# Performance work log

Hardware: AMD Instinct MI355X
Metric: run time of the kernel (lower is better)

## Reference

```python
import jax, jax.numpy as jnp
import numpy as np

TEMPERATURE = 0.1  # use_temperature=True


def setup_inputs() -> dict:
    key = jax.random.key(0)
    # encoder output features: [batch_size, num_epoch, feature_dim]
    feature = jax.random.normal(key, (128, 64, 128), dtype=jnp.float32)
    return {"feature": feature}


def reference(feature):
    # L2-normalize along feature dim (F.normalize, p=2, dim=1 on flat features)
    f = feature / jnp.linalg.norm(feature, axis=-1, keepdims=True)
    B, E, D = f.shape
    # full pairwise logits: [B, E, E, B]
    logits = jnp.einsum('ijk,mnk->ijnm', f, f) / TEMPERATURE
    e = jnp.exp(logits)
    idx = jnp.arange(B)
    # mask[i, j, :, i] = 1 -> positives are the m == i block: e[i, j, :, i]
    pos = e[idx, :, :, idx].sum(-1)              # [B, E]
    neg = e.sum(axis=(2, 3)) - pos               # [B, E] everything else
    loss = (-jnp.log(pos / (pos + neg))).mean()
    return loss
```

## Files before the change

kernel.cpp:

```cpp
#include <hip/hip_runtime.h>
#include <hip/hip_bf16.h>

#define N_ROWS 8192
#define DIM    128
#define TILE   128
#define CPG    8
#define EXPTEN 22026.465794806718f
#define SCALE  3.7982826f

typedef __attribute__((ext_vector_type(8))) short short8;
typedef __attribute__((ext_vector_type(4))) float floatx4;

#define EXP2F(x) __builtin_amdgcn_exp2f(x)

#define GLOAD_LDS(g, l)                                                        \
    __builtin_amdgcn_global_load_lds(                                          \
        (const __attribute__((address_space(1))) void*)(g),                    \
        (__attribute__((address_space(3))) void*)(l), 16, 0, 0)

__global__ void norm_kernel(const float* __restrict__ F, __hip_bfloat16* __restrict__ Xb,
                            float* __restrict__ pos, float* __restrict__ den) {
    int lane = threadIdx.x & 63;
    int wave = threadIdx.x >> 6;
    int row  = blockIdx.x * 4 + wave;
    const float2 v = *(const float2*)(F + (size_t)row * DIM + lane * 2);
    float ss = v.x * v.x + v.y * v.y;
    #pragma unroll
    for (int m = 1; m < 64; m <<= 1) ss += __shfl_xor(ss, m);
    float inv = rsqrtf(ss) * SCALE;
    __hip_bfloat162 o;
    o.x = __float2bfloat16(v.x * inv);
    o.y = __float2bfloat16(v.y * inv);
    *((__hip_bfloat162*)(Xb + (size_t)row * DIM) + lane) = o;
    if (lane == 0) { pos[row] = 0.f; den[row] = 0.f; }
}

__global__ __launch_bounds__(256, 2) void gram_kernel(
        const __hip_bfloat16* __restrict__ Xb,
        float* __restrict__ pos, float* __restrict__ den) {
    __shared__ __hip_bfloat16 Bs[2][TILE * DIM];
    const int tid  = threadIdx.x;
    const int rb   = blockIdx.x;
    const int cg   = blockIdx.y;
    const int lane = tid & 63;
    const int wave = tid >> 6;
    const int wm   = wave >> 1, wn = wave & 1;
    const int quad = lane >> 4;
    const int l15  = lane & 15;

    short8 af[4][4];
    {
        const __hip_bfloat16* Ab = Xb + ((size_t)(rb * TILE + wm * 64 + l15)) * DIM + quad * 8;
        #pragma unroll
        for (int mi = 0; mi < 4; ++mi)
            #pragma unroll
            for (int ko = 0; ko < 4; ++ko)
                af[mi][ko] = *(const short8*)(Ab + mi * 16 * DIM + ko * 32);
    }

    float dp[4][4];
    #pragma unroll
    for (int a = 0; a < 4; ++a)
        #pragma unroll
        for (int b = 0; b < 4; ++b) dp[a][b] = 0.f;

    auto stage = [&](int ct, int buf) {
        #pragma unroll
        for (int i = 0; i < 8; ++i) {
            int chunk = (i * 4 + wave) * 64 + lane;
            int r  = chunk >> 4;
            int cs = (chunk & 15) ^ (r & 15);
            const __hip_bfloat16* gp = Xb + ((size_t)(ct * TILE + r)) * DIM + cs * 8;
            char* lp = (char*)&Bs[buf][0] + (i * 4 + wave) * 1024;
            GLOAD_LDS(gp, lp);
        }
    };

    auto compute = [&](int ct, int buf) {
        floatx4 acc[4][4];
        #pragma unroll
        for (int mi = 0; mi < 4; ++mi)
            #pragma unroll
            for (int ni = 0; ni < 4; ++ni) acc[mi][ni] = (floatx4)0.0f;

        const char* Bb = (const char*)&Bs[buf][0];
        #pragma unroll
        for (int ko = 0; ko < 4; ++ko) {
            short8 bf[4];
            #pragma unroll
            for (int ni = 0; ni < 4; ++ni) {
                int r  = wn * 64 + ni * 16 + l15;
                int ch = (ko * 4 + quad) ^ l15;
                bf[ni] = *(const short8*)(Bb + r * 256 + ch * 16);
            }
            #pragma unroll
            for (int mi = 0; mi < 4; ++mi)
                #pragma unroll
                for (int ni = 0; ni < 4; ++ni)
                    acc[mi][ni] = __builtin_amdgcn_mfma_f32_16x16x32_bf16(
                        af[mi][ko], bf[ni], acc[mi][ni], 0, 0, 0);
        }

        const bool pos_tile = (ct == rb) && (wm == wn);
        #pragma unroll
        for (int mi = 0; mi < 4; ++mi)
            #pragma unroll
            for (int rg = 0; rg < 4; ++rg) {
                float dadd = 0.f;
                #pragma unroll
                for (int ni = 0; ni < 4; ++ni)
                    dadd += EXP2F(acc[mi][ni][rg]);
                if (pos_tile) {
                    if (l15 == quad * 4 + rg)
                        dadd += EXPTEN - EXP2F(acc[mi][mi][rg]);
                    float p = dadd;
                    #pragma unroll
                    for (int m = 1; m < 16; m <<= 1) p += __shfl_xor(p, m);
                    if (l15 == 0)
                        atomicAdd(&pos[rb * TILE + wm * 64 + mi * 16 + quad * 4 + rg], p);
                }
                dp[mi][rg] += dadd;
            }
    };

    stage(cg * CPG, 0);
    __syncthreads();
    #pragma unroll 1
    for (int t = 0; t < CPG - 1; ++t) {
        stage(cg * CPG + t + 1, (t + 1) & 1);
        compute(cg * CPG + t, t & 1);
        __syncthreads();
    }
    compute(cg * CPG + CPG - 1, (CPG - 1) & 1);

    #pragma unroll
    for (int mi = 0; mi < 4; ++mi)
        #pragma unroll
        for (int rg = 0; rg < 4; ++rg) {
            float d = dp[mi][rg];
            #pragma unroll
            for (int m = 1; m < 16; m <<= 1) d += __shfl_xor(d, m);
            if (l15 == 0)
                atomicAdd(&den[rb * TILE + wm * 64 + mi * 16 + quad * 4 + rg], d);
        }
}

__global__ void loss_kernel(const float* __restrict__ pos, const float* __restrict__ den,
                            float* __restrict__ out) {
    __shared__ float red[4];
    float acc = 0.f;
    for (int i = threadIdx.x; i < N_ROWS / 4; i += 256) {
        float4 d = ((const float4*)den)[i];
        float4 p = ((const float4*)pos)[i];
        acc += __logf(d.x / p.x) + __logf(d.y / p.y) +
               __logf(d.z / p.z) + __logf(d.w / p.w);
    }
    #pragma unroll
    for (int m = 1; m < 64; m <<= 1) acc += __shfl_xor(acc, m);
    int lane = threadIdx.x & 63, w = threadIdx.x >> 6;
    if (lane == 0) red[w] = acc;
    __syncthreads();
    if (threadIdx.x == 0)
        out[0] = (red[0] + red[1] + red[2] + red[3]) * (1.0f / (float)N_ROWS);
}

extern "C" void kernel_launch(void* const* d_in, const int* in_sizes, int n_in,
                              void* d_out, int out_size, void* d_ws, size_t ws_size,
                              hipStream_t stream) {
    const float* feature = (const float*)d_in[0];
    float* pos = (float*)d_ws;
    float* den = pos + N_ROWS;
    __hip_bfloat16* Xb = (__hip_bfloat16*)(den + N_ROWS);

    norm_kernel<<<N_ROWS / 4, 256, 0, stream>>>(feature, Xb, pos, den);
    gram_kernel<<<dim3(64, 8), 256, 0, stream>>>(Xb, pos, den);
    loss_kernel<<<1, 256, 0, stream>>>(pos, den, (float*)d_out);
}
```

Measured before the change: 87.69 us.

## Retile gram kernel to 256-row blocks with 64-column tiles and uneven split

The gram kernel now has each block hold 256 rows of A, one 64-row strip per wave, and stream 64-column B tiles through a smaller LDS double buffer. The 128 column tiles are split across 24 column groups of 5 or 6 tiles, giving 768 blocks. Launch bounds are raised to allow three blocks per CU. The aim is more A reuse per staged B tile, less LDS per block and better occupancy and load balance across the 256 CUs, at the cost of fewer MFMAs per sync and a slightly uneven per-block workload.

```diff
diff --git a/kernel.cpp b/kernel.cpp
--- a/kernel.cpp
+++ b/kernel.cpp
@@ -3,8 +3,6 @@
 
 #define N_ROWS 8192
 #define DIM    128
-#define TILE   128
-#define CPG    8
 #define EXPTEN 22026.465794806718f
 #define SCALE  3.7982826f
 
@@ -35,22 +33,25 @@
     if (lane == 0) { pos[row] = 0.f; den[row] = 0.f; }
 }
 
-__global__ __launch_bounds__(256, 2) void gram_kernel(
+__global__ __launch_bounds__(256, 3) void gram_kernel(
         const __hip_bfloat16* __restrict__ Xb,
         float* __restrict__ pos, float* __restrict__ den) {
-    __shared__ __hip_bfloat16 Bs[2][TILE * DIM];
+    __shared__ __hip_bfloat16 Bs[2][64 * DIM];
     const int tid  = threadIdx.x;
     const int rb   = blockIdx.x;
     const int cg   = blockIdx.y;
     const int lane = tid & 63;
     const int wave = tid >> 6;
-    const int wm   = wave >> 1, wn = wave & 1;
     const int quad = lane >> 4;
     const int l15  = lane & 15;
 
+    const int start = (cg < 16) ? cg * 5 : 80 + (cg - 16) * 6;
+    const int cnt   = (cg < 16) ? 5 : 6;
+
     short8 af[4][4];
     {
-        const __hip_bfloat16* Ab = Xb + ((size_t)(rb * TILE + wm * 64 + l15)) * DIM + quad * 8;
+        const __hip_bfloat16* Ab =
+            Xb + ((size_t)(rb * 256 + wave * 64 + l15)) * DIM + quad * 8;
         #pragma unroll
         for (int mi = 0; mi < 4; ++mi)
             #pragma unroll
@@ -66,11 +67,11 @@
 
     auto stage = [&](int ct, int buf) {
         #pragma unroll
-        for (int i = 0; i < 8; ++i) {
+        for (int i = 0; i < 4; ++i) {
             int chunk = (i * 4 + wave) * 64 + lane;
-            int r  = chunk >> 4;
-            int cs = (chunk & 15) ^ (r & 15);
-            const __hip_bfloat16* gp = Xb + ((size_t)(ct * TILE + r)) * DIM + cs * 8;
+            int c  = chunk >> 4;
+            int cs = (chunk & 15) ^ (c & 15);
+            const __hip_bfloat16* gp = Xb + ((size_t)(ct * 64 + c)) * DIM + cs * 8;
             char* lp = (char*)&Bs[buf][0] + (i * 4 + wave) * 1024;
             GLOAD_LDS(gp, lp);
         }
@@ -89,9 +90,9 @@
             short8 bf[4];
             #pragma unroll
             for (int ni = 0; ni < 4; ++ni) {
-                int r  = wn * 64 + ni * 16 + l15;
+                int c  = ni * 16 + l15;
                 int ch = (ko * 4 + quad) ^ l15;
-                bf[ni] = *(const short8*)(Bb + r * 256 + ch * 16);
+                bf[ni] = *(const short8*)(Bb + c * 256 + ch * 16);
             }
             #pragma unroll
             for (int mi = 0; mi < 4; ++mi)
@@ -101,7 +102,7 @@
                         af[mi][ko], bf[ni], acc[mi][ni], 0, 0, 0);
         }
 
-        const bool pos_tile = (ct == rb) && (wm == wn);
+        const bool pos_tile = (ct == rb * 4 + wave);
         #pragma unroll
         for (int mi = 0; mi < 4; ++mi)
             #pragma unroll
@@ -117,21 +118,21 @@
                     #pragma unroll
                     for (int m = 1; m < 16; m <<= 1) p += __shfl_xor(p, m);
                     if (l15 == 0)
-                        atomicAdd(&pos[rb * TILE + wm * 64 + mi * 16 + quad * 4 + rg], p);
+                        atomicAdd(&pos[rb * 256 + wave * 64 + mi * 16 + quad * 4 + rg], p);
                 }
                 dp[mi][rg] += dadd;
             }
     };
 
-    stage(cg * CPG, 0);
+    stage(start, 0);
     __syncthreads();
     #pragma unroll 1
-    for (int t = 0; t < CPG - 1; ++t) {
-        stage(cg * CPG + t + 1, (t + 1) & 1);
-        compute(cg * CPG + t, t & 1);
+    for (int t = 0; t < cnt - 1; ++t) {
+        stage(start + t + 1, (t + 1) & 1);
+        compute(start + t, t & 1);
         __syncthreads();
     }
-    compute(cg * CPG + CPG - 1, (CPG - 1) & 1);
+    compute(start + cnt - 1, (cnt - 1) & 1);
 
     #pragma unroll
     for (int mi = 0; mi < 4; ++mi)
@@ -141,7 +142,7 @@
             #pragma unroll
             for (int m = 1; m < 16; m <<= 1) d += __shfl_xor(d, m);
             if (l15 == 0)
-                atomicAdd(&den[rb * TILE + wm * 64 + mi * 16 + quad * 4 + rg], d);
+                atomicAdd(&den[rb * 256 + wave * 64 + mi * 16 + quad * 4 + rg], d);
         }
 }
 
@@ -149,11 +150,11 @@
                             float* __restrict__ out) {
     __shared__ float red[4];
     float acc = 0.f;
-    for (int i = threadIdx.x; i < N_ROWS / 4; i += 256) {
-        float4 d = ((const float4*)den)[i];
-        float4 p = ((const float4*)pos)[i];
-        acc += __logf(d.x / p.x) + __logf(d.y / p.y) +
-               __logf(d.z / p.z) + __logf(d.w / p.w);
+    for (int ii = threadIdx.x; ii < N_ROWS / 4; ii += 256) {
+        float4 dv = ((const float4*)den)[ii];
+        float4 pv = ((const float4*)pos)[ii];
+        acc += __logf(dv.x / pv.x) + __logf(dv.y / pv.y) +
+               __logf(dv.z / pv.z) + __logf(dv.w / pv.w);
     }
     #pragma unroll
     for (int m = 1; m < 64; m <<= 1) acc += __shfl_xor(acc, m);
@@ -173,6 +174,6 @@
     __hip_bfloat16* Xb = (__hip_bfloat16*)(den + N_ROWS);
 
     norm_kernel<<<N_ROWS / 4, 256, 0, stream>>>(feature, Xb, pos, den);
-    gram_kernel<<<dim3(64, 8), 256, 0, stream>>>(Xb, pos, den);
+    gram_kernel<<<dim3(32, 24), 256, 0, stream>>>(Xb, pos, den);
     loss_kernel<<<1, 256, 0, stream>>>(pos, den, (float*)d_out);
 }
```

New measurement: 133.5 us. +52.2%, slower.
